# Optimization experiments

Hardware: AMD Instinct MI355X
Metric: run time of the kernel (lower is better)

Reference implementation:

```python
import math
import jax, jax.numpy as jnp
import numpy as np

NEG = -1000000000.0


def setup_inputs() -> dict:
    key = jax.random.key(0)
    kq, kk, kv, km = jax.random.split(key, 4)
    B, H, S, D = 4, 16, 2048, 128
    q = jax.random.normal(kq, (B, H, S, D), dtype=jnp.float32)
    k = jax.random.normal(kk, (B, H, S, D), dtype=jnp.float32)
    v = jax.random.normal(kv, (B, H, S, D), dtype=jnp.float32)
    mask = jax.random.randint(km, (B, 1, 1, S), 0, 2, dtype=jnp.int32)
    return {"q": q, "k": k, "v": v, "mask": mask}


def reference(q, k, v, mask):
    # q,k,v: [B,H,S,D]; mask: [B,1,1,S] with 0 = masked out
    d_k = q.shape[-1]
    scores = jnp.einsum("bhqd,bhkd->bhqk", q, k) / math.sqrt(d_k)
    # additive padding mask (mask==0 -> -1e9)
    scores = scores + jnp.where(mask == 0, NEG, 0.0).astype(scores.dtype)
    # causal future mask (mask_future=True): strict upper triangle -> -1e9
    Qn, Kn = scores.shape[-2], scores.shape[-1]
    future = jnp.triu(jnp.ones((Qn, Kn), dtype=bool), k=1)
    scores = scores + jnp.where(future, NEG, 0.0).astype(scores.dtype)
    attn = jax.nn.softmax(scores, axis=-1)
    return jnp.einsum("bhqk,bhkd->bhqd", attn, v)
```

## Files before the change

### kernel.cpp

```cpp
#include <hip/hip_runtime.h>

typedef unsigned short u16;
typedef unsigned int   u32;
typedef __attribute__((ext_vector_type(8)))  short short8;
typedef __attribute__((ext_vector_type(4)))  float floatx4;
typedef __attribute__((ext_vector_type(16))) float floatx16;

#define CNEG  (-1.4426950408889634e9f)
#define QSCL  (0.12753129020334545f)
#define NEGF  (-1000000000.0f)
#define DEFER_THR 8.0f

__device__ __forceinline__ u16 f2bf(float x) {
  u32 u = __builtin_bit_cast(u32, x);
  u += 0x7fffu + ((u >> 16) & 1u);
  return (u16)(u >> 16);
}
__device__ __forceinline__ u32 cvtpk(float lo, float hi) {
  u32 r;
  asm("v_cvt_pk_bf16_f32 %0, %1, %2" : "=v"(r) : "v"(lo), "v"(hi));
  return r;
}

__device__ __forceinline__ int swzK(int r, int c)  { return r * 128 + (c ^ ((r & 7) << 3)); }
__device__ __forceinline__ int svb(int d)          { return ((d & 7) ^ ((d >> 2) & 7)) << 3; }
__device__ __forceinline__ int swzV(int d, int kv) { return d * 64 + (kv ^ svb(d)); }
__device__ __forceinline__ int swap23(int x) {
  return (x & ~0xC) | ((x & 4) << 1) | ((x & 8) >> 1);
}

__device__ __forceinline__ void gld16(const void* g, void* l) {
  __builtin_amdgcn_global_load_lds(
      (const __attribute__((address_space(1))) u32*)g,
      (__attribute__((address_space(3))) u32*)l, 16, 0, 0);
}

constexpr int Hh = 16, Ss = 2048, Dd = 128;
constexpr int KVBLK = 64;
constexpr int NT = Ss / KVBLK;
constexpr int TILE = KVBLK * Dd;
constexpr int NELEM = 4 * Hh * Ss * Dd;
constexpr int MASKN = 4 * Ss;

__global__ __launch_bounds__(256) void prep_kv(const float* __restrict__ K,
                                               const float* __restrict__ V,
                                               const int* __restrict__ MSK,
                                               u16* __restrict__ Kp, u16* __restrict__ Vp,
                                               float* __restrict__ Mg,
                                               float* __restrict__ Sp) {
  __shared__ u16 Vl[KVBLK * 132];
  const int blk = blockIdx.x, tid = threadIdx.x;
  const float* kg = K + (size_t)blk * TILE;
  const float* vg = V + (size_t)blk * TILE;
  u16* kp = Kp + (size_t)blk * TILE;
  u16* vp = Vp + (size_t)blk * TILE;

  if (blk < MASKN / 256) {
    int i = blk * 256 + tid;
    Mg[i] = MSK[i] ? 0.0f : CNEG;
  }

  #pragma unroll
  for (int it = 0; it < 4; ++it) {
    int ch = tid + it * 256;
    int f = ch >> 6, ln = ch & 63;
    int kvb = f >> 3, s = f & 7;
    int kvs = kvb * 32 + swap23(ln & 31);
    int d0 = s * 16 + (ln >> 5) * 8;
    const float* src = kg + kvs * 128 + d0;
    float4 a = *(const float4*)src, bq = *(const float4*)(src + 4);
    union { short8 v; u16 h[8]; } u;
    u.h[0] = f2bf(a.x);  u.h[1] = f2bf(a.y);  u.h[2] = f2bf(a.z);  u.h[3] = f2bf(a.w);
    u.h[4] = f2bf(bq.x); u.h[5] = f2bf(bq.y); u.h[6] = f2bf(bq.z); u.h[7] = f2bf(bq.w);
    *(short8*)(kp + ch * 8) = u.v;
  }
  #pragma unroll
  for (int it = 0; it < 8; ++it) {
    int e = (tid + it * 256) * 4;
    int r = e >> 7, c = e & 127;
    float4 a = *(const float4*)(vg + e);
    uint2 w;
    w.x = (u32)f2bf(a.x) | ((u32)f2bf(a.y) << 16);
    w.y = (u32)f2bf(a.z) | ((u32)f2bf(a.w) << 16);
    *(uint2*)&Vl[r * 132 + c] = w;
  }
  __syncthreads();
  #pragma unroll
  for (int it = 0; it < 4; ++it) {
    int ch = tid + it * 256;
    int f = ch >> 6, ln = ch & 63;
    int dt = f >> 2, s = f & 3;
    int d = dt * 32 + (ln & 31);
    int kv0 = s * 16 + (ln >> 5) * 8;
    union { short8 v; u16 h[8]; } u;
    #pragma unroll
    for (int i = 0; i < 8; ++i) u.h[i] = Vl[(kv0 + i) * 132 + d];
    *(short8*)(vp + ch * 8) = u.v;
  }

  {
    const int d = tid & 127, hf = tid >> 7;
    const int bb = blk >> 9;
    const int j0 = (blk & 31) * 64 + hf * 32;
    float acc = 0.0f;
    #pragma unroll 4
    for (int jj = 0; jj < 32; ++jj) {
      const float mfv = MSK[bb * Ss + j0 + jj] ? 1.0f : 0.0f;
      acc = fmaf(mfv, vg[(hf * 32 + jj) * 128 + d], acc);
    }
    __syncthreads();
    float* sred = (float*)Vl;
    if (hf) sred[d] = acc;
    __syncthreads();
    if (!hf) Sp[(size_t)blk * 128 + d] = acc + sred[d];
  }
}

__global__ __launch_bounds__(256) void mask_scan(const int* __restrict__ MSK,
                                                 int* __restrict__ F1M1) {
  __shared__ int sf[4], sc[4];
  const int b = blockIdx.x, tid = threadIdx.x, lane = tid & 63, wid = tid >> 6;
  int first = Ss, cnt = 0;
  for (int j = tid; j < Ss; j += 256)
    if (MSK[b * Ss + j]) { if (j < first) first = j; cnt++; }
  #pragma unroll
  for (int off = 1; off < 64; off <<= 1) {
    first = min(first, __shfl_xor(first, off, 64));
    cnt  += __shfl_xor(cnt, off, 64);
  }
  if (lane == 0) { sf[wid] = first; sc[wid] = cnt; }
  __syncthreads();
  if (tid == 0) {
    int f = min(min(sf[0], sf[1]), min(sf[2], sf[3]));
    int c = sc[0] + sc[1] + sc[2] + sc[3];
    F1M1[b] = f; F1M1[4 + b] = c;
  }
}

__global__ __launch_bounds__(128) void fixup(const float* __restrict__ V,
                                             const float* __restrict__ Sp,
                                             const int* __restrict__ F1M1,
                                             float* __restrict__ O) {
  const int bh = blockIdx.x, b = bh >> 4, d = threadIdx.x;
  const int f1 = F1M1[b];
  if (f1 == 0) return;
  const int m1 = F1M1[4 + b];
  float s1v = 0.0f;
  #pragma unroll
  for (int t = 0; t < NT; ++t) s1v += Sp[((size_t)bh * NT + t) * 128 + d];
  float pref = 0.0f;
  for (int i = 0; i < f1; ++i) {
    pref += V[((size_t)bh * Ss + i) * Dd + d];
    O[((size_t)bh * Ss + i) * Dd + d] = (pref + s1v) / (float)(i + 1 + m1);
  }
}

__global__ __launch_bounds__(256, 3) void attn_fwd(const float* __restrict__ Q,
                                                   const u16* __restrict__ Kp,
                                                   const u16* __restrict__ Vp,
                                                   const float* __restrict__ Mg,
                                                   float* __restrict__ O) {
  __shared__ u16 Kl[TILE];
  __shared__ u16 Vt[TILE];

  const int tid = threadIdx.x, lane = tid & 63, wid = tid >> 6;
  const int l31 = lane & 31, h = lane >> 5;
  const int id = blockIdx.x;
  const int wg = (id & 7) * 64 + (id >> 3);
  const int bh = wg >> 3, pr = wg & 7, b = bh >> 4;

  const size_t tb = (size_t)bh * NT;
  auto stage = [&](int t) {
    const char* gk = (const char*)(Kp + (tb + t) * TILE) + wid * 1024 + lane * 16;
    const char* gv = (const char*)(Vp + (tb + t) * TILE) + wid * 1024 + lane * 16;
    char* lk = (char*)&Kl[0] + wid * 1024;
    char* lv = (char*)&Vt[0] + wid * 1024;
    #pragma unroll
    for (int i = 0; i < 4; ++i) {
      gld16(gk + i * 4096, lk + i * 4096);
      gld16(gv + i * 4096, lv + i * 4096);
    }
  };

  #pragma unroll 1
  for (int strip = 0; strip < 2; ++strip) {
    const int qt = strip ? (15 - pr) : pr;
    const int qbase = qt * 128;
    const int nT = 2 * qt + 2;
    const int qi = qbase + wid * 32 + l31;

    const float* qg = Q + ((size_t)bh * Ss + qi) * Dd + h * 8;
    short8 qf[8];
    #pragma unroll
    for (int s = 0; s < 8; ++s) {
      float4 x0 = *(const float4*)(qg + s * 16);
      float4 x1 = *(const float4*)(qg + s * 16 + 4);
      union { short8 v; u16 hh[8]; } u;
      u.hh[0] = f2bf(x0.x * QSCL); u.hh[1] = f2bf(x0.y * QSCL);
      u.hh[2] = f2bf(x0.z * QSCL); u.hh[3] = f2bf(x0.w * QSCL);
      u.hh[4] = f2bf(x1.x * QSCL); u.hh[5] = f2bf(x1.y * QSCL);
      u.hh[6] = f2bf(x1.z * QSCL); u.hh[7] = f2bf(x1.w * QSCL);
      qf[s] = u.v;
    }

    float m_run = -3.0e38f, l_part = 0.0f;
    floatx16 oacc[4];
    #pragma unroll
    for (int dt = 0; dt < 4; ++dt)
      #pragma unroll
      for (int r = 0; r < 16; ++r) oacc[dt][r] = 0.0f;

    #pragma unroll 1
    for (int t = 0; t < nT; ++t) {
      __syncthreads();
      stage(t);
      __syncthreads();

      const int kvbase = t * KVBLK;

      const float* mrow = Mg + b * Ss + kvbase + h * 8;
      float4 a0 = *(const float4*)(mrow);
      float4 a1 = *(const float4*)(mrow + 4);
      float4 a2 = *(const float4*)(mrow + 16);
      float4 a3 = *(const float4*)(mrow + 20);
      float4 a4 = *(const float4*)(mrow + 32);
      float4 a5 = *(const float4*)(mrow + 36);
      float4 a6 = *(const float4*)(mrow + 48);
      float4 a7 = *(const float4*)(mrow + 52);
      floatx16 s0, s1;
      s0[0]=a0.x;  s0[1]=a0.y;  s0[2]=a0.z;  s0[3]=a0.w;
      s0[4]=a1.x;  s0[5]=a1.y;  s0[6]=a1.z;  s0[7]=a1.w;
      s0[8]=a2.x;  s0[9]=a2.y;  s0[10]=a2.z; s0[11]=a2.w;
      s0[12]=a3.x; s0[13]=a3.y; s0[14]=a3.z; s0[15]=a3.w;
      s1[0]=a4.x;  s1[1]=a4.y;  s1[2]=a4.z;  s1[3]=a4.w;
      s1[4]=a5.x;  s1[5]=a5.y;  s1[6]=a5.z;  s1[7]=a5.w;
      s1[8]=a6.x;  s1[9]=a6.y;  s1[10]=a6.z; s1[11]=a6.w;
      s1[12]=a7.x; s1[13]=a7.y; s1[14]=a7.z; s1[15]=a7.w;
      if (kvbase + KVBLK - 1 >= qbase + wid * 32) {
        #pragma unroll
        for (int r = 0; r < 16; ++r) {
          const int j0 = kvbase + ((r >> 3) << 4) + h * 8 + (r & 7);
          if (j0 > qi)      s0[r] += CNEG;
          if (j0 + 32 > qi) s1[r] += CNEG;
        }
      }

      const u16* kb = &Kl[lane * 8];
      __builtin_amdgcn_s_setprio(1);
      #pragma unroll
      for (int s = 0; s < 8; ++s) {
        short8 k0 = *(const short8*)&kb[s * 512];
        short8 k1 = *(const short8*)&kb[(8 + s) * 512];
        s0 = __builtin_amdgcn_mfma_f32_32x32x16_bf16(k0, qf[s], s0, 0, 0, 0);
        s1 = __builtin_amdgcn_mfma_f32_32x32x16_bf16(k1, qf[s], s1, 0, 0, 0);
      }
      __builtin_amdgcn_s_setprio(0);

      float mx8[8];
      #pragma unroll
      for (int r = 0; r < 8; ++r)
        mx8[r] = fmaxf(fmaxf(s0[r], s0[r + 8]), fmaxf(s1[r], s1[r + 8]));
      float mx4[4];
      #pragma unroll
      for (int r = 0; r < 4; ++r) mx4[r] = fmaxf(mx8[r], mx8[r + 4]);
      float pmax = fmaxf(fmaxf(mx4[0], mx4[1]), fmaxf(mx4[2], mx4[3]));

      float mn = m_run;
      if (!__all(pmax <= m_run + DEFER_THR)) {
        pmax = fmaxf(pmax, __shfl_xor(pmax, 32, 64));
        mn = fmaxf(m_run, pmax);
        const float alpha = exp2f(m_run - mn);
        m_run = mn;
        l_part *= alpha;
        #pragma unroll
        for (int dt = 0; dt < 4; ++dt)
          #pragma unroll
          for (int r = 0; r < 16; ++r) oacc[dt][r] *= alpha;
      }
      #pragma unroll
      for (int r = 0; r < 16; ++r) {
        const float p0 = exp2f(s0[r] - mn);
        const float p1 = exp2f(s1[r] - mn);
        s0[r] = p0; s1[r] = p1;
        l_part += p0 + p1;
      }

      union { short8 v; u32 w[4]; } pu[4];
      #pragma unroll
      for (int j = 0; j < 4; ++j) {
        pu[0].w[j] = cvtpk(s0[2 * j],     s0[2 * j + 1]);
        pu[1].w[j] = cvtpk(s0[8 + 2 * j], s0[8 + 2 * j + 1]);
        pu[2].w[j] = cvtpk(s1[2 * j],     s1[2 * j + 1]);
        pu[3].w[j] = cvtpk(s1[8 + 2 * j], s1[8 + 2 * j + 1]);
      }

      const u16* vb = &Vt[lane * 8];
      __builtin_amdgcn_s_setprio(1);
      #pragma unroll
      for (int ss = 0; ss < 4; ++ss) {
        #pragma unroll
        for (int dt = 0; dt < 4; ++dt) {
          short8 vf = *(const short8*)&vb[(dt * 4 + ss) * 512];
          oacc[dt] = __builtin_amdgcn_mfma_f32_32x32x16_bf16(vf, pu[ss].v, oacc[dt], 0, 0, 0);
        }
      }
      __builtin_amdgcn_s_setprio(0);
    }

    float l_run = l_part + __shfl_xor(l_part, 32, 64);
    const float inv = 1.0f / l_run;
    float* orow = O + ((size_t)bh * Ss + qi) * Dd;
    #pragma unroll
    for (int dt = 0; dt < 4; ++dt) {
      #pragma unroll
      for (int r32 = 0; r32 < 4; ++r32) {
        float4 o4;
        o4.x = oacc[dt][4 * r32 + 0] * inv;
        o4.y = oacc[dt][4 * r32 + 1] * inv;
        o4.z = oacc[dt][4 * r32 + 2] * inv;
        o4.w = oacc[dt][4 * r32 + 3] * inv;
        *(float4*)(orow + dt * 32 + 8 * r32 + 4 * h) = o4;
      }
    }
  }
}

__device__ __forceinline__ int swzPf(int row, int col) { return row * 64 + (col ^ ((row & 7) << 3)); }

__global__ __launch_bounds__(256) void attn_fb(
    const float* __restrict__ Q, const float* __restrict__ K,
    const float* __restrict__ V, const int* __restrict__ MSK,
    float* __restrict__ O)
{
  __shared__ u16 Kls[KVBLK * Dd];
  __shared__ u16 Vts[Dd * KVBLK];
  __shared__ u16 Pls[4][16 * KVBLK];
  __shared__ int sAff;

  const int tid = threadIdx.x, lane = tid & 63, wid = tid >> 6;
  const int l15 = lane & 15, lg = lane >> 4;
  const int qt = blockIdx.x, bh = blockIdx.y, b = bh >> 4;
  const int qbase = qt * 64;
  const float scale = 0.08838834764831845f;

  const int qrowA = qbase + wid * 16 + l15;
  const float* qg = Q + ((size_t)bh * Ss + qrowA) * Dd + lg * 8;
  short8 qf[4];
  #pragma unroll
  for (int kc = 0; kc < 4; ++kc) {
    float4 x0 = *(const float4*)(qg + kc * 32);
    float4 x1 = *(const float4*)(qg + kc * 32 + 4);
    union { short8 v; u16 h[8]; } u;
    u.h[0] = f2bf(x0.x * scale); u.h[1] = f2bf(x0.y * scale);
    u.h[2] = f2bf(x0.z * scale); u.h[3] = f2bf(x0.w * scale);
    u.h[4] = f2bf(x1.x * scale); u.h[5] = f2bf(x1.y * scale);
    u.h[6] = f2bf(x1.z * scale); u.h[7] = f2bf(x1.w * scale);
    qf[kc] = u.v;
  }

  float m_run[4], l_run[4];
  floatx4 oacc[8];
  const floatx4 vzero = {0.f, 0.f, 0.f, 0.f};
  #pragma unroll
  for (int r = 0; r < 4; ++r) { m_run[r] = -3.0e38f; l_run[r] = 0.0f; }
  #pragma unroll
  for (int dt = 0; dt < 8; ++dt) oacc[dt] = vzero;
  const int qi0 = qbase + wid * 16 + lg * 4;

  for (int t = 0; t < NT; ++t) {
    if (t > blockIdx.x && !sAff) break;
    const int kvbase = t * KVBLK;
    const float* kg = K + ((size_t)bh * Ss + kvbase) * Dd;
    const float* vg = V + ((size_t)bh * Ss + kvbase) * Dd;
    #pragma unroll
    for (int it = 0; it < 8; ++it) {
      int e = (tid + it * 256) * 4;
      int r0 = e >> 7, c0 = e & 127;
      float4 x = *(const float4*)(kg + e);
      uint2 hk;
      hk.x = (u32)f2bf(x.x) | ((u32)f2bf(x.y) << 16);
      hk.y = (u32)f2bf(x.z) | ((u32)f2bf(x.w) << 16);
      *(uint2*)&Kls[swzK(r0, c0)] = hk;
      float4 y = *(const float4*)(vg + e);
      u16 hv[4] = { f2bf(y.x), f2bf(y.y), f2bf(y.z), f2bf(y.w) };
      #pragma unroll
      for (int j = 0; j < 4; ++j) Vts[swzV(c0 + j, r0)] = hv[j];
    }
    __syncthreads();

    float madd[4];
    #pragma unroll
    for (int kt = 0; kt < 4; ++kt)
      madd[kt] = MSK[b * Ss + kvbase + kt * 16 + l15] ? 0.0f : NEGF;

    floatx4 sacc[4];
    #pragma unroll
    for (int kt = 0; kt < 4; ++kt) sacc[kt] = vzero;
    #pragma unroll
    for (int kt = 0; kt < 4; ++kt) {
      const int krow = kt * 16 + l15;
      #pragma unroll
      for (int kc = 0; kc < 4; ++kc) {
        short8 kf = *(const short8*)&Kls[swzK(krow, kc * 32 + lg * 8)];
        sacc[kt] = __builtin_amdgcn_mfma_f32_16x16x32_bf16(qf[kc], kf, sacc[kt], 0, 0, 0);
      }
    }

    float mnew[4];
    #pragma unroll
    for (int r = 0; r < 4; ++r) mnew[r] = m_run[r];
    #pragma unroll
    for (int kt = 0; kt < 4; ++kt) {
      const int kvj = kvbase + kt * 16 + l15;
      #pragma unroll
      for (int r = 0; r < 4; ++r) {
        float s = sacc[kt][r] + madd[kt];
        if (kvj > qi0 + r) s += NEGF;
        sacc[kt][r] = s;
        mnew[r] = fmaxf(mnew[r], s);
      }
    }
    #pragma unroll
    for (int off = 1; off < 16; off <<= 1) {
      #pragma unroll
      for (int r = 0; r < 4; ++r)
        mnew[r] = fmaxf(mnew[r], __shfl_xor(mnew[r], off, 64));
    }
    float alpha[4], psum[4];
    #pragma unroll
    for (int r = 0; r < 4; ++r) {
      alpha[r] = __expf(m_run[r] - mnew[r]);
      m_run[r] = mnew[r];
      psum[r] = 0.f;
    }
    #pragma unroll
    for (int kt = 0; kt < 4; ++kt) {
      #pragma unroll
      for (int r = 0; r < 4; ++r) {
        float p = __expf(sacc[kt][r] - mnew[r]);
        psum[r] += p;
        Pls[wid][swzPf(lg * 4 + r, kt * 16 + l15)] = f2bf(p);
      }
    }
    #pragma unroll
    for (int off = 1; off < 16; off <<= 1) {
      #pragma unroll
      for (int r = 0; r < 4; ++r)
        psum[r] += __shfl_xor(psum[r], off, 64);
    }
    #pragma unroll
    for (int r = 0; r < 4; ++r) l_run[r] = l_run[r] * alpha[r] + psum[r];
    #pragma unroll
    for (int dt = 0; dt < 8; ++dt) {
      #pragma unroll
      for (int r = 0; r < 4; ++r) oacc[dt][r] *= alpha[r];
    }
    #pragma unroll
    for (int kc = 0; kc < 2; ++kc) {
      short8 pfr = *(const short8*)&Pls[wid][swzPf(l15, kc * 32 + lg * 8)];
      #pragma unroll
      for (int dt = 0; dt < 8; ++dt) {
        short8 vf = *(const short8*)&Vts[swzV(dt * 16 + l15, kc * 32 + lg * 8)];
        oacc[dt] = __builtin_amdgcn_mfma_f32_16x16x32_bf16(pfr, vf, oacc[dt], 0, 0, 0);
      }
    }
    __syncthreads();

    if (t == blockIdx.x) {
      if (tid == 0) sAff = 0;
      __syncthreads();
      bool aff = (m_run[0] < -5.0e8f) || (m_run[1] < -5.0e8f) ||
                 (m_run[2] < -5.0e8f) || (m_run[3] < -5.0e8f);
      if (aff) sAff = 1;
      __syncthreads();
    }
  }

  #pragma unroll
  for (int r = 0; r < 4; ++r) {
    float inv = 1.0f / l_run[r];
    float* op = O + ((size_t)bh * Ss + qi0 + r) * Dd + l15;
    #pragma unroll
    for (int dt = 0; dt < 8; ++dt) op[dt * 16] = oacc[dt][r] * inv;
  }
}

extern "C" void kernel_launch(void* const* d_in, const int* in_sizes, int n_in,
                              void* d_out, int out_size, void* d_ws, size_t ws_size,
                              hipStream_t stream) {
  const float* q = (const float*)d_in[0];
  const float* k = (const float*)d_in[1];
  const float* v = (const float*)d_in[2];
  const int* mask = (const int*)d_in[3];
  float* out = (float*)d_out;

  const size_t need = (size_t)2 * NELEM * sizeof(u16)
                    + (size_t)MASKN * sizeof(float)
                    + (size_t)64 * NT * 128 * sizeof(float)
                    + 8 * sizeof(int);
  if (ws_size >= need) {
    u16* Kp = (u16*)d_ws;
    u16* Vp = Kp + NELEM;
    float* Mg = (float*)(Vp + NELEM);
    float* Sp = Mg + MASKN;
    int* F1M1 = (int*)(Sp + (size_t)64 * NT * 128);
    prep_kv<<<dim3(64 * NT), 256, 0, stream>>>(k, v, mask, Kp, Vp, Mg, Sp);
    mask_scan<<<dim3(4), 256, 0, stream>>>(mask, F1M1);
    attn_fwd<<<dim3(512), 256, 0, stream>>>(q, Kp, Vp, Mg, out);
    fixup<<<dim3(64), 128, 0, stream>>>(v, Sp, F1M1, out);
  } else {
    attn_fb<<<dim3(NT, 64), 256, 0, stream>>>(q, k, v, mask, out);
  }
}
```

Before: 190.5 us.

## Double-buffer K tiles and launch one Q tile per block, heaviest first

The K shared-memory tile becomes double-buffered, so the next K tile is fetched while the current QK^T runs, and V staging is issued early and waited on just before the PV matmuls. Each block now handles a single query tile, ordered heaviest-first, instead of a balanced pair of causal strips, which doubles the grid to 1024 blocks. This hides global-to-LDS latency and leaves load balancing to the hardware scheduler, at the cost of extra LDS per block (which may lower occupancy) and losing the explicit pairwise balancing.

```diff
diff --git a/kernel.cpp b/kernel.cpp
--- a/kernel.cpp
+++ b/kernel.cpp
@@ -160,167 +160,172 @@
                                                    const u16* __restrict__ Vp,
                                                    const float* __restrict__ Mg,
                                                    float* __restrict__ O) {
-  __shared__ u16 Kl[TILE];
+  __shared__ u16 Kl[2][TILE];
   __shared__ u16 Vt[TILE];
 
   const int tid = threadIdx.x, lane = tid & 63, wid = tid >> 6;
   const int l31 = lane & 31, h = lane >> 5;
   const int id = blockIdx.x;
-  const int wg = (id & 7) * 64 + (id >> 3);
-  const int bh = wg >> 3, pr = wg & 7, b = bh >> 4;
+  const int wg = (id & 7) * 128 + (id >> 3);
+  const int bh = wg >> 4, b = bh >> 4;
+  const int qt = 15 - (wg & 15);
+  const int qbase = qt * 128;
+  const int nT = 2 * qt + 2;
+  const int qi = qbase + wid * 32 + l31;
 
   const size_t tb = (size_t)bh * NT;
-  auto stage = [&](int t) {
+  auto stageK = [&](int buf, int t) {
     const char* gk = (const char*)(Kp + (tb + t) * TILE) + wid * 1024 + lane * 16;
+    char* lk = (char*)&Kl[buf][0] + wid * 1024;
+    #pragma unroll
+    for (int i = 0; i < 4; ++i) gld16(gk + i * 4096, lk + i * 4096);
+  };
+  auto stageV = [&](int t) {
     const char* gv = (const char*)(Vp + (tb + t) * TILE) + wid * 1024 + lane * 16;
-    char* lk = (char*)&Kl[0] + wid * 1024;
     char* lv = (char*)&Vt[0] + wid * 1024;
     #pragma unroll
-    for (int i = 0; i < 4; ++i) {
-      gld16(gk + i * 4096, lk + i * 4096);
-      gld16(gv + i * 4096, lv + i * 4096);
-    }
+    for (int i = 0; i < 4; ++i) gld16(gv + i * 4096, lv + i * 4096);
   };
 
+  const float* qg = Q + ((size_t)bh * Ss + qi) * Dd + h * 8;
+  short8 qf[8];
+  #pragma unroll
+  for (int s = 0; s < 8; ++s) {
+    float4 x0 = *(const float4*)(qg + s * 16);
+    float4 x1 = *(const float4*)(qg + s * 16 + 4);
+    union { short8 v; u16 hh[8]; } u;
+    u.hh[0] = f2bf(x0.x * QSCL); u.hh[1] = f2bf(x0.y * QSCL);
+    u.hh[2] = f2bf(x0.z * QSCL); u.hh[3] = f2bf(x0.w * QSCL);
+    u.hh[4] = f2bf(x1.x * QSCL); u.hh[5] = f2bf(x1.y * QSCL);
+    u.hh[6] = f2bf(x1.z * QSCL); u.hh[7] = f2bf(x1.w * QSCL);
+    qf[s] = u.v;
+  }
+
+  float m_run = -3.0e38f, l_part = 0.0f;
+  floatx16 oacc[4];
+  #pragma unroll
+  for (int dt = 0; dt < 4; ++dt)
+    #pragma unroll
+    for (int r = 0; r < 16; ++r) oacc[dt][r] = 0.0f;
+
+  stageK(0, 0);
+  __syncthreads();
+  int cur = 0;
+
   #pragma unroll 1
-  for (int strip = 0; strip < 2; ++strip) {
-    const int qt = strip ? (15 - pr) : pr;
-    const int qbase = qt * 128;
-    const int nT = 2 * qt + 2;
-    const int qi = qbase + wid * 32 + l31;
-
-    const float* qg = Q + ((size_t)bh * Ss + qi) * Dd + h * 8;
-    short8 qf[8];
+  for (int t = 0; t < nT; ++t) {
+    stageV(t);
+    if (t + 1 < nT) stageK(cur ^ 1, t + 1);
+
+    const int kvbase = t * KVBLK;
+
+    const float* mrow = Mg + b * Ss + kvbase + h * 8;
+    float4 a0 = *(const float4*)(mrow);
+    float4 a1 = *(const float4*)(mrow + 4);
+    float4 a2 = *(const float4*)(mrow + 16);
+    float4 a3 = *(const float4*)(mrow + 20);
+    float4 a4 = *(const float4*)(mrow + 32);
+    float4 a5 = *(const float4*)(mrow + 36);
+    float4 a6 = *(const float4*)(mrow + 48);
+    float4 a7 = *(const float4*)(mrow + 52);
+    floatx16 s0, s1;
+    s0[0]=a0.x;  s0[1]=a0.y;  s0[2]=a0.z;  s0[3]=a0.w;
+    s0[4]=a1.x;  s0[5]=a1.y;  s0[6]=a1.z;  s0[7]=a1.w;
+    s0[8]=a2.x;  s0[9]=a2.y;  s0[10]=a2.z; s0[11]=a2.w;
+    s0[12]=a3.x; s0[13]=a3.y; s0[14]=a3.z; s0[15]=a3.w;
+    s1[0]=a4.x;  s1[1]=a4.y;  s1[2]=a4.z;  s1[3]=a4.w;
+    s1[4]=a5.x;  s1[5]=a5.y;  s1[6]=a5.z;  s1[7]=a5.w;
+    s1[8]=a6.x;  s1[9]=a6.y;  s1[10]=a6.z; s1[11]=a6.w;
+    s1[12]=a7.x; s1[13]=a7.y; s1[14]=a7.z; s1[15]=a7.w;
+    if (kvbase + KVBLK - 1 >= qbase + wid * 32) {
+      #pragma unroll
+      for (int r = 0; r < 16; ++r) {
+        const int j0 = kvbase + ((r >> 3) << 4) + h * 8 + (r & 7);
+        if (j0 > qi)      s0[r] += CNEG;
+        if (j0 + 32 > qi) s1[r] += CNEG;
+      }
+    }
+
+    const u16* kb = &Kl[cur][lane * 8];
+    __builtin_amdgcn_s_setprio(1);
     #pragma unroll
     for (int s = 0; s < 8; ++s) {
-      float4 x0 = *(const float4*)(qg + s * 16);
-      float4 x1 = *(const float4*)(qg + s * 16 + 4);
-      union { short8 v; u16 hh[8]; } u;
-      u.hh[0] = f2bf(x0.x * QSCL); u.hh[1] = f2bf(x0.y * QSCL);
-      u.hh[2] = f2bf(x0.z * QSCL); u.hh[3] = f2bf(x0.w * QSCL);
-      u.hh[4] = f2bf(x1.x * QSCL); u.hh[5] = f2bf(x1.y * QSCL);
-      u.hh[6] = f2bf(x1.z * QSCL); u.hh[7] = f2bf(x1.w * QSCL);
-      qf[s] = u.v;
-    }
-
-    float m_run = -3.0e38f, l_part = 0.0f;
-    floatx16 oacc[4];
-    #pragma unroll
-    for (int dt = 0; dt < 4; ++dt)
-      #pragma unroll
-      for (int r = 0; r < 16; ++r) oacc[dt][r] = 0.0f;
-
-    #pragma unroll 1
-    for (int t = 0; t < nT; ++t) {
-      __syncthreads();
-      stage(t);
-      __syncthreads();
-
-      const int kvbase = t * KVBLK;
-
-      const float* mrow = Mg + b * Ss + kvbase + h * 8;
-      float4 a0 = *(const float4*)(mrow);
-      float4 a1 = *(const float4*)(mrow + 4);
-      float4 a2 = *(const float4*)(mrow + 16);
-      float4 a3 = *(const float4*)(mrow + 20);
-      float4 a4 = *(const float4*)(mrow + 32);
-      float4 a5 = *(const float4*)(mrow + 36);
-      float4 a6 = *(const float4*)(mrow + 48);
-      float4 a7 = *(const float4*)(mrow + 52);
-      floatx16 s0, s1;
-      s0[0]=a0.x;  s0[1]=a0.y;  s0[2]=a0.z;  s0[3]=a0.w;
-      s0[4]=a1.x;  s0[5]=a1.y;  s0[6]=a1.z;  s0[7]=a1.w;
-      s0[8]=a2.x;  s0[9]=a2.y;  s0[10]=a2.z; s0[11]=a2.w;
-      s0[12]=a3.x; s0[13]=a3.y; s0[14]=a3.z; s0[15]=a3.w;
-      s1[0]=a4.x;  s1[1]=a4.y;  s1[2]=a4.z;  s1[3]=a4.w;
-      s1[4]=a5.x;  s1[5]=a5.y;  s1[6]=a5.z;  s1[7]=a5.w;
-      s1[8]=a6.x;  s1[9]=a6.y;  s1[10]=a6.z; s1[11]=a6.w;
-      s1[12]=a7.x; s1[13]=a7.y; s1[14]=a7.z; s1[15]=a7.w;
-      if (kvbase + KVBLK - 1 >= qbase + wid * 32) {
+      short8 k0 = *(const short8*)&kb[s * 512];
+      short8 k1 = *(const short8*)&kb[(8 + s) * 512];
+      s0 = __builtin_amdgcn_mfma_f32_32x32x16_bf16(k0, qf[s], s0, 0, 0, 0);
+      s1 = __builtin_amdgcn_mfma_f32_32x32x16_bf16(k1, qf[s], s1, 0, 0, 0);
+    }
+    __builtin_amdgcn_s_setprio(0);
+
+    float mx8[8];
+    #pragma unroll
+    for (int r = 0; r < 8; ++r)
+      mx8[r] = fmaxf(fmaxf(s0[r], s0[r + 8]), fmaxf(s1[r], s1[r + 8]));
+    float mx4[4];
+    #pragma unroll
+    for (int r = 0; r < 4; ++r) mx4[r] = fmaxf(mx8[r], mx8[r + 4]);
+    float pmax = fmaxf(fmaxf(mx4[0], mx4[1]), fmaxf(mx4[2], mx4[3]));
+
+    float mn = m_run;
+    if (!__all(pmax <= m_run + DEFER_THR)) {
+      pmax = fmaxf(pmax, __shfl_xor(pmax, 32, 64));
+      mn = fmaxf(m_run, pmax);
+      const float alpha = exp2f(m_run - mn);
+      m_run = mn;
+      l_part *= alpha;
+      #pragma unroll
+      for (int dt = 0; dt < 4; ++dt)
         #pragma unroll
-        for (int r = 0; r < 16; ++r) {
-          const int j0 = kvbase + ((r >> 3) << 4) + h * 8 + (r & 7);
-          if (j0 > qi)      s0[r] += CNEG;
-          if (j0 + 32 > qi) s1[r] += CNEG;
-        }
+        for (int r = 0; r < 16; ++r) oacc[dt][r] *= alpha;
+    }
+    #pragma unroll
+    for (int r = 0; r < 16; ++r) {
+      const float p0 = exp2f(s0[r] - mn);
+      const float p1 = exp2f(s1[r] - mn);
+      s0[r] = p0; s1[r] = p1;
+      l_part += p0 + p1;
+    }
+
+    union { short8 v; u32 w[4]; } pu[4];
+    #pragma unroll
+    for (int j = 0; j < 4; ++j) {
+      pu[0].w[j] = cvtpk(s0[2 * j],     s0[2 * j + 1]);
+      pu[1].w[j] = cvtpk(s0[8 + 2 * j], s0[8 + 2 * j + 1]);
+      pu[2].w[j] = cvtpk(s1[2 * j],     s1[2 * j + 1]);
+      pu[3].w[j] = cvtpk(s1[8 + 2 * j], s1[8 + 2 * j + 1]);
+    }
+
+    __syncthreads();
+
+    const u16* vb = &Vt[lane * 8];
+    __builtin_amdgcn_s_setprio(1);
+    #pragma unroll
+    for (int ss = 0; ss < 4; ++ss) {
+      #pragma unroll
+      for (int dt = 0; dt < 4; ++dt) {
+        short8 vf = *(const short8*)&vb[(dt * 4 + ss) * 512];
+        oacc[dt] = __builtin_amdgcn_mfma_f32_32x32x16_bf16(vf, pu[ss].v, oacc[dt], 0, 0, 0);
       }
-
-      const u16* kb = &Kl[lane * 8];
-      __builtin_amdgcn_s_setprio(1);
-      #pragma unroll
-      for (int s = 0; s < 8; ++s) {
-        short8 k0 = *(const short8*)&kb[s * 512];
-        short8 k1 = *(const short8*)&kb[(8 + s) * 512];
-        s0 = __builtin_amdgcn_mfma_f32_32x32x16_bf16(k0, qf[s], s0, 0, 0, 0);
-        s1 = __builtin_amdgcn_mfma_f32_32x32x16_bf16(k1, qf[s], s1, 0, 0, 0);
-      }
-      __builtin_amdgcn_s_setprio(0);
-
-      float mx8[8];
-      #pragma unroll
-      for (int r = 0; r < 8; ++r)
-        mx8[r] = fmaxf(fmaxf(s0[r], s0[r + 8]), fmaxf(s1[r], s1[r + 8]));
-      float mx4[4];
-      #pragma unroll
-      for (int r = 0; r < 4; ++r) mx4[r] = fmaxf(mx8[r], mx8[r + 4]);
-      float pmax = fmaxf(fmaxf(mx4[0], mx4[1]), fmaxf(mx4[2], mx4[3]));
-
-      float mn = m_run;
-      if (!__all(pmax <= m_run + DEFER_THR)) {
-        pmax = fmaxf(pmax, __shfl_xor(pmax, 32, 64));
-        mn = fmaxf(m_run, pmax);
-        const float alpha = exp2f(m_run - mn);
-        m_run = mn;
-        l_part *= alpha;
-        #pragma unroll
-        for (int dt = 0; dt < 4; ++dt)
-          #pragma unroll
-          for (int r = 0; r < 16; ++r) oacc[dt][r] *= alpha;
-      }
-      #pragma unroll
-      for (int r = 0; r < 16; ++r) {
-        const float p0 = exp2f(s0[r] - mn);
-        const float p1 = exp2f(s1[r] - mn);
-        s0[r] = p0; s1[r] = p1;
-        l_part += p0 + p1;
-      }
-
-      union { short8 v; u32 w[4]; } pu[4];
-      #pragma unroll
-      for (int j = 0; j < 4; ++j) {
-        pu[0].w[j] = cvtpk(s0[2 * j],     s0[2 * j + 1]);
-        pu[1].w[j] = cvtpk(s0[8 + 2 * j], s0[8 + 2 * j + 1]);
-        pu[2].w[j] = cvtpk(s1[2 * j],     s1[2 * j + 1]);
-        pu[3].w[j] = cvtpk(s1[8 + 2 * j], s1[8 + 2 * j + 1]);
-      }
-
-      const u16* vb = &Vt[lane * 8];
-      __builtin_amdgcn_s_setprio(1);
-      #pragma unroll
-      for (int ss = 0; ss < 4; ++ss) {
-        #pragma unroll
-        for (int dt = 0; dt < 4; ++dt) {
-          short8 vf = *(const short8*)&vb[(dt * 4 + ss) * 512];
-          oacc[dt] = __builtin_amdgcn_mfma_f32_32x32x16_bf16(vf, pu[ss].v, oacc[dt], 0, 0, 0);
-        }
-      }
-      __builtin_amdgcn_s_setprio(0);
-    }
-
-    float l_run = l_part + __shfl_xor(l_part, 32, 64);
-    const float inv = 1.0f / l_run;
-    float* orow = O + ((size_t)bh * Ss + qi) * Dd;
-    #pragma unroll
-    for (int dt = 0; dt < 4; ++dt) {
-      #pragma unroll
-      for (int r32 = 0; r32 < 4; ++r32) {
-        float4 o4;
-        o4.x = oacc[dt][4 * r32 + 0] * inv;
-        o4.y = oacc[dt][4 * r32 + 1] * inv;
-        o4.z = oacc[dt][4 * r32 + 2] * inv;
-        o4.w = oacc[dt][4 * r32 + 3] * inv;
-        *(float4*)(orow + dt * 32 + 8 * r32 + 4 * h) = o4;
-      }
+    }
+    __builtin_amdgcn_s_setprio(0);
+
+    __syncthreads();
+    cur ^= 1;
+  }
+
+  float l_run = l_part + __shfl_xor(l_part, 32, 64);
+  const float inv = 1.0f / l_run;
+  float* orow = O + ((size_t)bh * Ss + qi) * Dd;
+  #pragma unroll
+  for (int dt = 0; dt < 4; ++dt) {
+    #pragma unroll
+    for (int r32 = 0; r32 < 4; ++r32) {
+      float4 o4;
+      o4.x = oacc[dt][4 * r32 + 0] * inv;
+      o4.y = oacc[dt][4 * r32 + 1] * inv;
+      o4.z = oacc[dt][4 * r32 + 2] * inv;
+      o4.w = oacc[dt][4 * r32 + 3] * inv;
+      *(float4*)(orow + dt * 32 + 8 * r32 + 4 * h) = o4;
     }
   }
 }
@@ -506,7 +511,7 @@
     int* F1M1 = (int*)(Sp + (size_t)64 * NT * 128);
     prep_kv<<<dim3(64 * NT), 256, 0, stream>>>(k, v, mask, Kp, Vp, Mg, Sp);
     mask_scan<<<dim3(4), 256, 0, stream>>>(mask, F1M1);
-    attn_fwd<<<dim3(512), 256, 0, stream>>>(q, Kp, Vp, Mg, out);
+    attn_fwd<<<dim3(1024), 256, 0, stream>>>(q, Kp, Vp, Mg, out);
     fixup<<<dim3(64), 128, 0, stream>>>(v, Sp, F1M1, out);
   } else {
     attn_fb<<<dim3(NT, 64), 256, 0, stream>>>(q, k, v, mask, out);
```

After: 199.2 us. 1.05x slower.
